# Performance work log

Hardware: AMD Instinct MI355X
Metric: run time of the kernel (lower is better)

Reference implementation:

```python
import jax, jax.numpy as jnp
import numpy as np

B, TS, TD = 32, 64, 63          # batch, src len, dec steps (dm_max_length_chinese-1)
VS, VT = 32000, 32000           # source/target vocab
E, U = 256, 1024                # embed dim, LSTM units


def _lstm_step(x_t, h, c, Wx, Wh, b):
    # Keras gate order: i, f, g(candidate), o
    z = x_t @ Wx + h @ Wh + b                      # [B, 4U]
    i, f, g, o = jnp.split(z, 4, axis=-1)
    c_new = jax.nn.sigmoid(f) * c + jax.nn.sigmoid(i) * jnp.tanh(g)
    h_new = jax.nn.sigmoid(o) * jnp.tanh(c_new)
    return h_new, c_new


def setup_inputs() -> dict:
    key = jax.random.key(0)
    ks = jax.random.split(key, 16)
    s_e = 1.0 / np.sqrt(E)
    s_u = 1.0 / np.sqrt(U)
    s_eu = 1.0 / np.sqrt(E + U)
    return {
        "encoder_input": jax.random.randint(ks[0], (B, TS), 0, VS, dtype=jnp.int32),
        "decoder_input": jax.random.randint(ks[1], (B, TD), 0, VT, dtype=jnp.int32),
        "enc_emb": jax.random.normal(ks[2], (VS, E), jnp.float32) * 0.02,
        "dec_emb": jax.random.normal(ks[3], (VT, E), jnp.float32) * 0.02,
        "Wx_e": jax.random.normal(ks[4], (E, 4 * U), jnp.float32) * s_e,
        "Wh_e": jax.random.normal(ks[5], (U, 4 * U), jnp.float32) * s_u,
        "b_e": jnp.zeros((4 * U,), jnp.float32),
        "Wx_d": jax.random.normal(ks[6], (E + U, 4 * U), jnp.float32) * s_eu,
        "Wh_d": jax.random.normal(ks[7], (U, 4 * U), jnp.float32) * s_u,
        "b_d": jnp.zeros((4 * U,), jnp.float32),
        "Wm": jax.random.normal(ks[8], (U, U), jnp.float32) * s_u,    # Luong memory layer (no bias)
        "Wa": jax.random.normal(ks[9], (2 * U, U), jnp.float32) * (1.0 / np.sqrt(2 * U)),  # attention layer (no bias)
        "Wf": jax.random.normal(ks[10], (U, VT), jnp.float32) * s_u,
        "bf": jnp.zeros((VT,), jnp.float32),
    }


def reference(encoder_input, decoder_input, enc_emb, dec_emb,
              Wx_e, Wh_e, b_e, Wx_d, Wh_d, b_d, Wm, Wa, Wf, bf):
    # ---- Encoder: Embedding + LSTM(return_sequences, return_state) ----
    enc_x = enc_emb[encoder_input]                          # [B, TS, E]

    def enc_step(carry, x_t):
        h, c = carry
        h, c = _lstm_step(x_t, h, c, Wx_e, Wh_e, b_e)
        return (h, c), h

    h0 = jnp.zeros((B, U), enc_x.dtype)
    (h_enc, c_enc), memory = jax.lax.scan(enc_step, (h0, h0),
                                          jnp.swapaxes(enc_x, 0, 1))
    memory = jnp.swapaxes(memory, 0, 1)                     # [B, TS, U]

    # Luong attention keys: memory_layer(memory)
    keys = jnp.einsum('bsu,uv->bsv', memory, Wm)            # [B, TS, U]

    # ---- Decoder: AttentionWrapper(LSTMCell) + output Dense, per step ----
    dec_x = dec_emb[decoder_input]                          # [B, TD, E]

    def dec_step(carry, x_t):
        h, c, attn = carry
        cell_in = jnp.concatenate([x_t, attn], axis=-1)     # [B, E+U]
        h, c = _lstm_step(cell_in, h, c, Wx_d, Wh_d, b_d)
        score = jnp.einsum('bu,bsu->bs', h, keys)           # Luong dot score
        align = jax.nn.softmax(score, axis=-1)              # full-length mask -> plain softmax
        context = jnp.einsum('bs,bsu->bu', align, memory)
        attn = jnp.concatenate([h, context], axis=-1) @ Wa  # attention layer, no bias
        logits = attn @ Wf + bf                             # output projection
        return (h, c, attn), logits

    attn0 = jnp.zeros((B, U), dec_x.dtype)
    _, logits = jax.lax.scan(dec_step, (h_enc, c_enc, attn0),
                             jnp.swapaxes(dec_x, 0, 1))
    return jnp.swapaxes(logits, 0, 1)                       # [B, TD, VT]
```

## Files before the change

### kernel.cpp

```cpp
#include <hip/hip_runtime.h>
#include <hip/hip_bf16.h>

#define B_  32
#define TS_ 64
#define TD_ 63
#define E_  256
#define U_  1024
#define G_  4096
#define VT_ 32000

typedef __attribute__((ext_vector_type(8))) short short8;
typedef __attribute__((ext_vector_type(4))) float floatx4;

__device__ __forceinline__ float sigf(float x){ return 1.0f/(1.0f+__expf(-x)); }
__device__ __forceinline__ float tanh_fast(float x){ return 2.0f/(1.0f+__expf(-2.0f*x)) - 1.0f; }
__device__ __forceinline__ unsigned short f2bf(float x){
  unsigned u = __float_as_uint(x);
  u += 0x7FFFu + ((u>>16)&1u);
  return (unsigned short)(u>>16);
}

__global__ void zero_kernel(float4* __restrict__ p, int n4){
  int i = blockIdx.x*256 + threadIdx.x;
  if(i < n4) p[i] = make_float4(0.f,0.f,0.f,0.f);
}

__global__ __launch_bounds__(256) void gemm_rows(
    const float* __restrict__ Atab, const int* __restrict__ tokens, int T,
    const float* __restrict__ Bw, const float* __restrict__ bias,
    float* __restrict__ C, int N, int K)
{
  __shared__ float as[64*20];
  int tid = threadIdx.x;
  int n  = blockIdx.x*256 + tid;
  int m0 = blockIdx.y*16;
  float acc[16];
  #pragma unroll
  for(int r=0;r<16;r++) acc[r]=0.f;

  for(int kc=0; kc<K; kc+=64){
    __syncthreads();
    for(int i=tid; i<16*64; i+=256){
      int mm = i>>6, kk = i&63;
      int m = m0 + mm;
      const float* arow;
      if(tokens){
        int b = m & 31, t = m >> 5;
        arow = Atab + (size_t)tokens[b*T + t]*K;
      } else {
        arow = Atab + (size_t)m*K;
      }
      as[kk*20 + mm] = arow[kc + kk];
    }
    __syncthreads();
    for(int kk=0; kk<64; kk++){
      float bv = Bw[(size_t)(kc+kk)*N + n];
      const float4* ap = (const float4*)(as + kk*20);
      float4 a0 = ap[0], a1 = ap[1], a2 = ap[2], a3 = ap[3];
      acc[0]  += a0.x*bv; acc[1]  += a0.y*bv; acc[2]  += a0.z*bv; acc[3]  += a0.w*bv;
      acc[4]  += a1.x*bv; acc[5]  += a1.y*bv; acc[6]  += a1.z*bv; acc[7]  += a1.w*bv;
      acc[8]  += a2.x*bv; acc[9]  += a2.y*bv; acc[10] += a2.z*bv; acc[11] += a2.w*bv;
      acc[12] += a3.x*bv; acc[13] += a3.y*bv; acc[14] += a3.z*bv; acc[15] += a3.w*bv;
    }
  }
  float bv = bias ? bias[n] : 0.f;
  #pragma unroll
  for(int r=0;r<16;r++)
    C[(size_t)(m0+r)*N + n] = acc[r] + bv;
}

__global__ __launch_bounds__(256) void step_mm(
    const float* __restrict__ W1, const float* __restrict__ W2,
    const float* __restrict__ s1, const float* __restrict__ s2,
    float* __restrict__ zpart, int N)
{
  int tid = threadIdx.x;
  int nl = tid & 63, mg = tid >> 6;
  int n = blockIdx.x*64 + nl;
  int kq = blockIdx.y;
  int k0 = (kq & 3) * 256;
  const float* W  = ((kq < 4) ? W1 : W2) + (size_t)k0 * N + n;
  const float* hp = ((kq < 4) ? s1 : s2) + (size_t)(mg*8) * U_ + k0;
  float acc[8];
  #pragma unroll
  for(int i=0;i<8;i++) acc[i]=0.f;
  #pragma unroll 4
  for(int k=0; k<256; k++){
    float wv = W[(size_t)k * N];
    #pragma unroll
    for(int mi=0; mi<8; mi++)
      acc[mi] += hp[(size_t)mi*U_ + k] * wv;
  }
  float* zp = zpart + ((size_t)(kq*32 + mg*8)) * N + n;
  #pragma unroll
  for(int mi=0; mi<8; mi++)
    zp[(size_t)mi * N] = acc[mi];
}

__global__ __launch_bounds__(256) void gate_h(
    const float* __restrict__ X_t, const float* __restrict__ zpart, int KQ,
    float* __restrict__ c, float* __restrict__ hout)
{
  int i = blockIdx.x*256 + threadIdx.x;
  int b = i >> 10, u = i & 1023;
  float zg[4];
  #pragma unroll
  for(int g=0; g<4; g++){
    int col = g*U_ + u;
    float s = X_t[(size_t)b*G_ + col];
    for(int p=0; p<KQ; p++) s += zpart[((size_t)(p*32+b))*G_ + col];
    zg[g] = s;
  }
  float cn = sigf(zg[1])*c[i] + sigf(zg[0])*tanh_fast(zg[2]);
  float hn = sigf(zg[3])*tanh_fast(cn);
  c[i] = cn;
  hout[i] = hn;
}

__global__ __launch_bounds__(256) void dec_gate_attn(
    const float* __restrict__ Xd_t, const float* __restrict__ zpart,
    float* __restrict__ c, const float* __restrict__ keys,
    const float* __restrict__ memory, float* __restrict__ hout,
    float* __restrict__ ctx)
{
  int b = blockIdx.x;
  int tid = threadIdx.x;
  __shared__ float hs[1024];
  __shared__ float sc[64];
  __shared__ float al[64];
  #pragma unroll
  for(int uu=0; uu<4; uu++){
    int u = uu*256 + tid;
    float zg[4];
    #pragma unroll
    for(int g=0; g<4; g++){
      int col = g*U_ + u;
      float s = Xd_t[(size_t)b*G_ + col];
      #pragma unroll
      for(int p=0; p<8; p++) s += zpart[((size_t)(p*32+b))*G_ + col];
      zg[g] = s;
    }
    int ci = b*U_ + u;
    float cn = sigf(zg[1])*c[ci] + sigf(zg[0])*tanh_fast(zg[2]);
    float hn = sigf(zg[3])*tanh_fast(cn);
    c[ci] = cn;
    hs[u] = hn;
    hout[ci] = hn;
  }
  __syncthreads();
  int w = tid>>6, lane = tid&63;
  for(int si=0; si<16; si++){
    int s = w*16 + si;
    const float* kr = keys + ((size_t)s*B_ + b)*U_;
    float p = 0.f;
    for(int kk=lane; kk<1024; kk+=64) p += hs[kk]*kr[kk];
    for(int off=32; off; off>>=1) p += __shfl_down(p, off);
    if(lane==0) sc[s] = p;
  }
  __syncthreads();
  if(tid<64){
    float v = sc[tid];
    float mx = v;
    for(int off=32; off; off>>=1) mx = fmaxf(mx, __shfl_down(mx, off));
    mx = __shfl(mx, 0);
    float e = __expf(v - mx);
    float sm = e;
    for(int off=32; off; off>>=1) sm += __shfl_down(sm, off);
    sm = __shfl(sm, 0);
    al[tid] = e/sm;
  }
  __syncthreads();
  #pragma unroll
  for(int uu=0; uu<4; uu++){
    int u = uu*256 + tid;
    float a = 0.f;
    for(int s=0; s<64; s++) a += al[s]*memory[((size_t)s*B_ + b)*U_ + u];
    ctx[b*U_ + u] = a;
  }
}

__global__ __launch_bounds__(256) void attn_combine(
    const float* __restrict__ apart, float* __restrict__ attn_next,
    unsigned short* __restrict__ abf)
{
  int i = blockIdx.x*256 + threadIdx.x;
  float s = 0.f;
  #pragma unroll
  for(int p=0; p<8; p++) s += apart[(size_t)p*32768 + i];
  attn_next[i] = s;
  abf[i] = f2bf(s);
}

__global__ __launch_bounds__(256) void transpose_f2bf(
    const float* __restrict__ Wf, unsigned short* __restrict__ WfT)
{
  __shared__ float t[32][33];
  int n0 = blockIdx.x*32, k0 = blockIdx.y*32;
  int tid = threadIdx.x;
  int cx = tid&31, ry = tid>>5;
  for(int r=ry; r<32; r+=8) t[r][cx] = Wf[(size_t)(k0+r)*VT_ + n0+cx];
  __syncthreads();
  for(int r=ry; r<32; r+=8)
    WfT[(size_t)(n0+r)*1024 + k0+cx] = f2bf(t[cx][r]);
}

__global__ __launch_bounds__(256) void logits_gemm(
    const unsigned short* __restrict__ Abf, const unsigned short* __restrict__ Bt,
    const float* __restrict__ bias, float* __restrict__ out)
{
  __shared__ __align__(16) unsigned short As[32][40];
  __shared__ __align__(16) unsigned short Bs[256][40];
  int tid = threadIdx.x;
  int m0 = blockIdx.x*32, n0 = blockIdx.y*256;
  int w = tid>>6, lane = tid&63;
  int wm = w&1, wn = w>>1;
  floatx4 acc[8];
  #pragma unroll
  for(int i=0;i<8;i++) acc[i] = (floatx4)(0.f);

  int rl = lane&15, kg = lane>>4;

  for(int kt=0; kt<1024; kt+=32){
    __syncthreads();
    {
      int mm = tid>>3, kq = tid&7;
      const unsigned short* src = Abf + (size_t)(m0+mm)*1024 + kt + kq*4;
      *(uint2*)(&As[mm][kq*4]) = *(const uint2*)src;
    }
    {
      const unsigned short* bsrc = Bt + (size_t)(n0+tid)*1024 + kt;
      *(uint4*)(&Bs[tid][0])  = *(const uint4*)(bsrc);
      *(uint4*)(&Bs[tid][8])  = *(const uint4*)(bsrc+8);
      *(uint4*)(&Bs[tid][16]) = *(const uint4*)(bsrc+16);
      *(uint4*)(&Bs[tid][24]) = *(const uint4*)(bsrc+24);
    }
    __syncthreads();
    short8 afrag = *(const short8*)(&As[wm*16 + rl][kg*8]);
    #pragma unroll
    for(int nt=0; nt<8; nt++){
      short8 bfrag = *(const short8*)(&Bs[wn*128 + nt*16 + rl][kg*8]);
      acc[nt] = __builtin_amdgcn_mfma_f32_16x16x32_bf16(afrag, bfrag, acc[nt], 0,0,0);
    }
  }
  #pragma unroll
  for(int nt=0; nt<8; nt++){
    int n = n0 + wn*128 + nt*16 + rl;
    float bv = bias[n];
    #pragma unroll
    for(int r=0;r<4;r++){
      int m = m0 + wm*16 + kg*4 + r;
      int t = m>>5, b = m&31;
      out[((size_t)(b*TD_) + t)*VT_ + n] = acc[nt][r] + bv;
    }
  }
}

extern "C" void kernel_launch(void* const* d_in, const int* in_sizes, int n_in,
                              void* d_out, int out_size, void* d_ws, size_t ws_size,
                              hipStream_t stream) {
  (void)in_sizes; (void)n_in; (void)out_size; (void)ws_size;
  const int*   enc_in  = (const int*)d_in[0];
  const int*   dec_in  = (const int*)d_in[1];
  const float* enc_emb = (const float*)d_in[2];
  const float* dec_emb = (const float*)d_in[3];
  const float* Wx_e    = (const float*)d_in[4];
  const float* Wh_e    = (const float*)d_in[5];
  const float* b_e     = (const float*)d_in[6];
  const float* Wx_d    = (const float*)d_in[7];
  const float* Wh_d    = (const float*)d_in[8];
  const float* b_d     = (const float*)d_in[9];
  const float* Wm      = (const float*)d_in[10];
  const float* Wa      = (const float*)d_in[11];
  const float* Wf      = (const float*)d_in[12];
  const float* bf      = (const float*)d_in[13];
  float* out = (float*)d_out;

  float* ws = (float*)d_ws;
  size_t off = 0;
  float* Xe       = ws + off; off += (size_t)TS_*B_*G_;
  float* Xd       = ws + off; off += (size_t)TD_*B_*G_;
  float* memory   = ws + off; off += (size_t)TS_*B_*U_;
  float* keys     = ws + off; off += (size_t)TS_*B_*U_;
  float* attn_buf = ws + off; off += (size_t)64*B_*U_;
  float* cbuf     = ws + off; off += (size_t)B_*U_;
  float* hbuf     = ws + off; off += (size_t)B_*U_;
  float* ctx      = ws + off; off += (size_t)B_*U_;
  float* zpart    = ws + off; off += (size_t)8*B_*G_;
  float* apart    = ws + off; off += (size_t)8*B_*U_;
  unsigned short* attn_bf = (unsigned short*)(ws + off); off += (size_t)(2016*1024)/2;
  unsigned short* WfT     = (unsigned short*)(ws + off);

  zero_kernel<<<32, 256, 0, stream>>>((float4*)attn_buf, (B_*U_)/4);
  zero_kernel<<<32, 256, 0, stream>>>((float4*)cbuf, (B_*U_)/4);

  gemm_rows<<<dim3(G_/256, (TS_*B_)/16), 256, 0, stream>>>(enc_emb, enc_in, TS_, Wx_e, b_e, Xe, G_, E_);
  gemm_rows<<<dim3(G_/256, (TD_*B_)/16), 256, 0, stream>>>(dec_emb, dec_in, TD_, Wx_d, b_d, Xd, G_, E_);
  transpose_f2bf<<<dim3(VT_/32, 1024/32), 256, 0, stream>>>(Wf, WfT);

  for(int t=0; t<TS_; t++){
    const float* hprev = (t==0) ? attn_buf : memory + (size_t)(t-1)*B_*U_;
    step_mm<<<dim3(G_/64, 4), 256, 0, stream>>>(Wh_e, Wh_e, hprev, hprev, zpart, G_);
    gate_h<<<128, 256, 0, stream>>>(Xe + (size_t)t*B_*G_, zpart, 4, cbuf,
                                    memory + (size_t)t*B_*U_);
  }

  gemm_rows<<<dim3(U_/256, (TS_*B_)/16), 256, 0, stream>>>(memory, nullptr, 0, Wm, nullptr, keys, U_, U_);

  const float* mem_last = memory + (size_t)(TS_-1)*B_*U_;
  const float* Wxa = Wx_d + (size_t)E_*G_;
  const float* Wa2 = Wa + (size_t)U_*U_;
  for(int t=0; t<TD_; t++){
    const float* hin   = (t==0) ? mem_last : hbuf;
    const float* aprev = attn_buf + (size_t)t*B_*U_;
    float* anext       = attn_buf + (size_t)(t+1)*B_*U_;
    step_mm<<<dim3(G_/64, 8), 256, 0, stream>>>(Wh_d, Wxa, hin, aprev, zpart, G_);
    dec_gate_attn<<<B_, 256, 0, stream>>>(Xd + (size_t)t*B_*G_, zpart, cbuf,
                                          keys, memory, hbuf, ctx);
    step_mm<<<dim3(U_/64, 8), 256, 0, stream>>>(Wa, Wa2, hbuf, ctx, apart, U_);
    attn_combine<<<128, 256, 0, stream>>>(apart, anext, attn_bf + (size_t)t*B_*U_);
  }

  logits_gemm<<<dim3((TD_*B_)/32, VT_/256), 256, 0, stream>>>(attn_bf, WfT, bf, out);
}
```

Baseline: 15.82 ms.

## Fuse encoder/decoder recurrence into one persistent cooperative kernel with grid syncs

Replaces the per-timestep launches of step_mm, gate_h, dec_gate_attn and attn_combine with a single cooperative kernel of 256 blocks. The kernel loops over encoder and decoder steps and uses grid.sync between phases, and it also computes the keys projection. The aim is to remove several hundred kernel launches and their gaps. In exchange it pays for grid-wide barriers, and some phases run on only 32 blocks while the others idle. If the cooperative launch fails, the code falls back to the old launch sequence.

New measurement: 41.15 ms. 2.6x slower.

```diff
diff --git a/kernel.cpp b/kernel.cpp
--- a/kernel.cpp
+++ b/kernel.cpp
@@ -1,5 +1,8 @@
 #include <hip/hip_runtime.h>
 #include <hip/hip_bf16.h>
+#include <hip/hip_cooperative_groups.h>
+
+namespace cg = cooperative_groups;
 
 #define B_  32
 #define TS_ 64
@@ -189,6 +192,213 @@
   for(int p=0; p<8; p++) s += apart[(size_t)p*32768 + i];
   attn_next[i] = s;
   abf[i] = f2bf(s);
+}
+
+struct RecParams {
+  const float* Xe; const float* Xd;
+  const float* Wh_e; const float* Wh_d; const float* Wxa;
+  const float* Wm; const float* Wa;
+  float* memory; float* keys; float* attn_buf;
+  float* cbuf; float* hbuf; float* ctx;
+  float* zpart;
+  float* apart;
+  unsigned short* attn_bf;
+};
+
+__global__ __launch_bounds__(256) void seq_rnn(RecParams P)
+{
+  cg::grid_group grid = cg::this_grid();
+  __shared__ float hs[1024];
+  __shared__ float sc[64];
+  __shared__ float al[64];
+  const int bid  = blockIdx.x;
+  const int tid  = threadIdx.x;
+  const int lane = tid & 63;
+  const int mg   = tid >> 6;
+
+  for(int t=0; t<TS_; ++t){
+    {
+      const float* hprev = (t==0) ? P.attn_buf : P.memory + (size_t)(t-1)*B_*U_;
+      const int nb = bid & 63, kq = bid >> 6;
+      const int n = nb*64 + lane, k0 = kq*256;
+      const float* W  = P.Wh_e + (size_t)k0*G_ + n;
+      const float* hp = hprev + (size_t)(mg*8)*U_ + k0;
+      float acc[8];
+      #pragma unroll
+      for(int i=0;i<8;i++) acc[i]=0.f;
+      #pragma unroll 4
+      for(int k=0;k<256;k++){
+        float wv = W[(size_t)k*G_];
+        #pragma unroll
+        for(int mi=0;mi<8;mi++) acc[mi] += hp[(size_t)mi*U_+k]*wv;
+      }
+      float* zp = P.zpart + ((size_t)(kq*32+mg*8))*G_ + n;
+      #pragma unroll
+      for(int mi=0;mi<8;mi++) zp[(size_t)mi*G_] = acc[mi];
+    }
+    grid.sync();
+    {
+      const int gidx = bid*256 + tid;
+      if(gidx < B_*U_){
+        const int b = gidx>>10, u = gidx&1023;
+        const float* Xt = P.Xe + (size_t)t*B_*G_ + (size_t)b*G_;
+        float zg[4];
+        #pragma unroll
+        for(int g=0;g<4;g++){
+          const int col = g*U_+u;
+          float s = Xt[col];
+          #pragma unroll
+          for(int p=0;p<4;p++) s += P.zpart[((size_t)(p*32+b))*G_+col];
+          zg[g]=s;
+        }
+        const float cn = sigf(zg[1])*P.cbuf[gidx] + sigf(zg[0])*tanh_fast(zg[2]);
+        const float hn = sigf(zg[3])*tanh_fast(cn);
+        P.cbuf[gidx]=cn;
+        P.memory[(size_t)t*B_*U_+gidx]=hn;
+      }
+    }
+    grid.sync();
+  }
+
+  {
+    const int nb = bid & 15, rq = bid >> 4;
+    const int n = nb*64 + lane;
+    for(int rg=0; rg<4; rg++){
+      const int r0 = rq*128 + rg*32 + mg*8;
+      const float* src = P.memory + (size_t)r0*U_;
+      float acc[8];
+      #pragma unroll
+      for(int i=0;i<8;i++) acc[i]=0.f;
+      #pragma unroll 4
+      for(int k=0;k<1024;k++){
+        float wv = P.Wm[(size_t)k*U_ + n];
+        #pragma unroll
+        for(int mi=0;mi<8;mi++) acc[mi] += src[(size_t)mi*U_+k]*wv;
+      }
+      float* kp = P.keys + (size_t)r0*U_ + n;
+      #pragma unroll
+      for(int mi=0;mi<8;mi++) kp[(size_t)mi*U_] = acc[mi];
+    }
+  }
+  grid.sync();
+
+  for(int t=0; t<TD_; ++t){
+    const float* hin   = (t==0) ? (P.memory + (size_t)(TS_-1)*B_*U_) : P.hbuf;
+    const float* aprev = P.attn_buf + (size_t)t*B_*U_;
+    {
+      const int nb = bid & 63, kq = bid >> 6;
+      const int n = nb*64 + lane, k0 = kq*256;
+      float acc[8];
+      #pragma unroll
+      for(int i=0;i<8;i++) acc[i]=0.f;
+      const float* W1 = P.Wh_d + (size_t)k0*G_ + n;
+      const float* h1 = hin + (size_t)(mg*8)*U_ + k0;
+      #pragma unroll 4
+      for(int k=0;k<256;k++){
+        float wv = W1[(size_t)k*G_];
+        #pragma unroll
+        for(int mi=0;mi<8;mi++) acc[mi] += h1[(size_t)mi*U_+k]*wv;
+      }
+      const float* W2 = P.Wxa + (size_t)k0*G_ + n;
+      const float* h2 = aprev + (size_t)(mg*8)*U_ + k0;
+      #pragma unroll 4
+      for(int k=0;k<256;k++){
+        float wv = W2[(size_t)k*G_];
+        #pragma unroll
+        for(int mi=0;mi<8;mi++) acc[mi] += h2[(size_t)mi*U_+k]*wv;
+      }
+      float* zp = P.zpart + ((size_t)(kq*32+mg*8))*G_ + n;
+      #pragma unroll
+      for(int mi=0;mi<8;mi++) zp[(size_t)mi*G_] = acc[mi];
+    }
+    grid.sync();
+    if(bid < B_){
+      const int b = bid;
+      const float* Xt = P.Xd + (size_t)t*B_*G_ + (size_t)b*G_;
+      #pragma unroll
+      for(int uu=0; uu<4; uu++){
+        const int u = uu*256 + tid;
+        float zg[4];
+        #pragma unroll
+        for(int g=0;g<4;g++){
+          const int col = g*U_+u;
+          float s = Xt[col];
+          #pragma unroll
+          for(int p=0;p<4;p++) s += P.zpart[((size_t)(p*32+b))*G_+col];
+          zg[g]=s;
+        }
+        const int ci = b*U_+u;
+        const float cn = sigf(zg[1])*P.cbuf[ci] + sigf(zg[0])*tanh_fast(zg[2]);
+        const float hn = sigf(zg[3])*tanh_fast(cn);
+        P.cbuf[ci]=cn; hs[u]=hn; P.hbuf[ci]=hn;
+      }
+      __syncthreads();
+      const int w = tid>>6, ln = tid&63;
+      for(int si=0; si<16; si++){
+        const int s = w*16 + si;
+        const float* kr = P.keys + ((size_t)s*B_ + b)*U_;
+        float p = 0.f;
+        for(int kk=ln; kk<1024; kk+=64) p += hs[kk]*kr[kk];
+        #pragma unroll
+        for(int off=32; off; off>>=1) p += __shfl_down(p, off);
+        if(ln==0) sc[s] = p;
+      }
+      __syncthreads();
+      if(tid<64){
+        float v = sc[tid];
+        float mx = v;
+        #pragma unroll
+        for(int off=32; off; off>>=1) mx = fmaxf(mx, __shfl_down(mx, off));
+        mx = __shfl(mx, 0);
+        float e = __expf(v - mx);
+        float sm = e;
+        #pragma unroll
+        for(int off=32; off; off>>=1) sm += __shfl_down(sm, off);
+        sm = __shfl(sm, 0);
+        al[tid] = e/sm;
+      }
+      __syncthreads();
+      #pragma unroll
+      for(int uu=0; uu<4; uu++){
+        const int u = uu*256 + tid;
+        float a = 0.f;
+        for(int s=0; s<64; s++) a += al[s]*P.memory[((size_t)s*B_ + b)*U_ + u];
+        P.ctx[b*U_+u] = a;
+      }
+    }
+    grid.sync();
+    {
+      const int nb = bid & 15, kq = bid >> 4;
+      const int n = nb*64 + lane;
+      const float* W = P.Wa + (size_t)(kq*128)*U_ + n;
+      const float* src = (kq < 8) ? (P.hbuf + (size_t)(mg*8)*U_ + kq*128)
+                                  : (P.ctx  + (size_t)(mg*8)*U_ + (kq-8)*128);
+      float acc[8];
+      #pragma unroll
+      for(int i=0;i<8;i++) acc[i]=0.f;
+      #pragma unroll 4
+      for(int k=0;k<128;k++){
+        float wv = W[(size_t)k*U_];
+        #pragma unroll
+        for(int mi=0;mi<8;mi++) acc[mi] += src[(size_t)mi*U_+k]*wv;
+      }
+      float* ap = P.apart + ((size_t)(kq*32+mg*8))*U_ + n;
+      #pragma unroll
+      for(int mi=0;mi<8;mi++) ap[(size_t)mi*U_] = acc[mi];
+    }
+    grid.sync();
+    {
+      const int gidx = bid*256 + tid;
+      if(gidx < B_*U_){
+        float s = 0.f;
+        #pragma unroll
+        for(int p=0;p<16;p++) s += P.apart[(size_t)p*B_*U_ + gidx];
+        P.attn_buf[(size_t)(t+1)*B_*U_ + gidx] = s;
+        P.attn_bf[(size_t)t*B_*U_ + gidx] = f2bf(s);
+      }
+    }
+    grid.sync();
+  }
 }
 
 __global__ __launch_bounds__(256) void transpose_f2bf(
@@ -297,27 +507,41 @@
   gemm_rows<<<dim3(G_/256, (TD_*B_)/16), 256, 0, stream>>>(dec_emb, dec_in, TD_, Wx_d, b_d, Xd, G_, E_);
   transpose_f2bf<<<dim3(VT_/32, 1024/32), 256, 0, stream>>>(Wf, WfT);
 
-  for(int t=0; t<TS_; t++){
-    const float* hprev = (t==0) ? attn_buf : memory + (size_t)(t-1)*B_*U_;
-    step_mm<<<dim3(G_/64, 4), 256, 0, stream>>>(Wh_e, Wh_e, hprev, hprev, zpart, G_);
-    gate_h<<<128, 256, 0, stream>>>(Xe + (size_t)t*B_*G_, zpart, 4, cbuf,
-                                    memory + (size_t)t*B_*U_);
-  }
-
-  gemm_rows<<<dim3(U_/256, (TS_*B_)/16), 256, 0, stream>>>(memory, nullptr, 0, Wm, nullptr, keys, U_, U_);
-
-  const float* mem_last = memory + (size_t)(TS_-1)*B_*U_;
   const float* Wxa = Wx_d + (size_t)E_*G_;
-  const float* Wa2 = Wa + (size_t)U_*U_;
-  for(int t=0; t<TD_; t++){
-    const float* hin   = (t==0) ? mem_last : hbuf;
-    const float* aprev = attn_buf + (size_t)t*B_*U_;
-    float* anext       = attn_buf + (size_t)(t+1)*B_*U_;
-    step_mm<<<dim3(G_/64, 8), 256, 0, stream>>>(Wh_d, Wxa, hin, aprev, zpart, G_);
-    dec_gate_attn<<<B_, 256, 0, stream>>>(Xd + (size_t)t*B_*G_, zpart, cbuf,
-                                          keys, memory, hbuf, ctx);
-    step_mm<<<dim3(U_/64, 8), 256, 0, stream>>>(Wa, Wa2, hbuf, ctx, apart, U_);
-    attn_combine<<<128, 256, 0, stream>>>(apart, anext, attn_bf + (size_t)t*B_*U_);
+
+  RecParams P;
+  P.Xe = Xe; P.Xd = Xd;
+  P.Wh_e = Wh_e; P.Wh_d = Wh_d; P.Wxa = Wxa;
+  P.Wm = Wm; P.Wa = Wa;
+  P.memory = memory; P.keys = keys; P.attn_buf = attn_buf;
+  P.cbuf = cbuf; P.hbuf = hbuf; P.ctx = ctx;
+  P.zpart = zpart;
+  P.apart = zpart + (size_t)4*B_*G_;
+  P.attn_bf = attn_bf;
+  void* kargs[1] = { (void*)&P };
+  hipError_t ce = hipLaunchCooperativeKernel(seq_rnn, dim3(256), dim3(256),
+                                             kargs, 0u, stream);
+
+  if(ce != hipSuccess){
+    for(int t=0; t<TS_; t++){
+      const float* hprev = (t==0) ? attn_buf : memory + (size_t)(t-1)*B_*U_;
+      step_mm<<<dim3(G_/64, 4), 256, 0, stream>>>(Wh_e, Wh_e, hprev, hprev, zpart, G_);
+      gate_h<<<128, 256, 0, stream>>>(Xe + (size_t)t*B_*G_, zpart, 4, cbuf,
+                                      memory + (size_t)t*B_*U_);
+    }
+    gemm_rows<<<dim3(U_/256, (TS_*B_)/16), 256, 0, stream>>>(memory, nullptr, 0, Wm, nullptr, keys, U_, U_);
+    const float* mem_last = memory + (size_t)(TS_-1)*B_*U_;
+    const float* Wa2 = Wa + (size_t)U_*U_;
+    for(int t=0; t<TD_; t++){
+      const float* hin   = (t==0) ? mem_last : hbuf;
+      const float* aprev = attn_buf + (size_t)t*B_*U_;
+      float* anext       = attn_buf + (size_t)(t+1)*B_*U_;
+      step_mm<<<dim3(G_/64, 8), 256, 0, stream>>>(Wh_d, Wxa, hin, aprev, zpart, G_);
+      dec_gate_attn<<<B_, 256, 0, stream>>>(Xd + (size_t)t*B_*G_, zpart, cbuf,
+                                            keys, memory, hbuf, ctx);
+      step_mm<<<dim3(U_/64, 8), 256, 0, stream>>>(Wa, Wa2, hbuf, ctx, apart, U_);
+      attn_combine<<<128, 256, 0, stream>>>(apart, anext, attn_bf + (size_t)t*B_*U_);
+    }
   }
 
   logits_gemm<<<dim3((TD_*B_)/32, VT_/256), 256, 0, stream>>>(attn_bf, WfT, bf, out);
```
